# Kernel optimization log

Measured on AMD Instinct MI355X. Metric: run time of the kernel, lower is better.

## Reference

```python
import jax, jax.numpy as jnp
import numpy as np

NODE_DIM = 128
DEPTH = 4
N_NODES = 10000
N_EDGES = 320000


def setup_inputs() -> dict:
    key = jax.random.key(0)
    ks = jax.random.split(key, 12)
    s = 0.05
    D = NODE_DIM
    inp = {
        'h': jax.random.normal(ks[0], (N_NODES, D), jnp.float32),
        'x': jax.random.normal(ks[1], (N_NODES, 3), jnp.float32),
        'edges': jax.random.randint(ks[2], (2, N_EDGES), 0, N_NODES, jnp.int32),
        # edge_mlp: Linear(2D+1 -> D), SiLU, Linear(D -> D), SiLU  (per layer)
        'edge_w1': jax.random.normal(ks[3], (DEPTH, 2 * D + 1, D), jnp.float32) * s,
        'edge_b1': jnp.zeros((DEPTH, D), jnp.float32),
        'edge_w2': jax.random.normal(ks[4], (DEPTH, D, D), jnp.float32) * s,
        'edge_b2': jnp.zeros((DEPTH, D), jnp.float32),
        # node_mlp: Linear(2D -> D), SiLU, Linear(D -> D)  (per layer)
        'node_w1': jax.random.normal(ks[5], (DEPTH, 2 * D, D), jnp.float32) * s,
        'node_b1': jnp.zeros((DEPTH, D), jnp.float32),
        'node_w2': jax.random.normal(ks[6], (DEPTH, D, D), jnp.float32) * s,
        'node_b2': jnp.zeros((DEPTH, D), jnp.float32),
        # coord_mlp (only used by last layer, update_coords=True):
        # Linear(D -> D), SiLU, Linear(D -> 1, bias=False)
        'coord_w1': jax.random.normal(ks[7], (D, D), jnp.float32) * s,
        'coord_b1': jnp.zeros((D,), jnp.float32),
        'coord_w2': jax.random.normal(ks[8], (D, 1), jnp.float32) * s,
    }
    return inp


def reference(h, x, edges, edge_w1, edge_b1, edge_w2, edge_b2,
              node_w1, node_b1, node_w2, node_b2,
              coord_w1, coord_b1, coord_w2):
    silu = jax.nn.silu
    row, col = edges[0], edges[1]
    n = h.shape[0]
    for i in range(DEPTH):
        # coord2radial
        coord_diff = x[row] - x[col]                       # [E, 3]
        radial = jnp.sum(coord_diff * coord_diff, axis=-1, keepdims=True)  # [E, 1]
        # edge_model: m_ij = edge_mlp([h_i, h_j, radial])
        feat = jnp.concatenate([h[row], h[col], radial], axis=-1)  # [E, 2D+1]
        m = silu(feat @ edge_w1[i] + edge_b1[i])
        m = silu(m @ edge_w2[i] + edge_b2[i])              # [E, D]
        # coord_model (only last layer, coords_agg='mean')
        if i == DEPTH - 1:
            w = silu(m @ coord_w1 + coord_b1) @ coord_w2   # [E, 1]
            trans = coord_diff * w                          # [E, 3]
            agg = jax.ops.segment_sum(trans, row, num_segments=n)
            cnt = jax.ops.segment_sum(jnp.ones((row.shape[0], 1), trans.dtype),
                                      row, num_segments=n)
            x = x + agg / jnp.maximum(cnt, 1.0)
        # node_model: h = h + node_mlp([h, sum_j m_ij])  (residual=True)
        magg = jax.ops.segment_sum(m, row, num_segments=n)  # [N, D]
        hin = jnp.concatenate([h, magg], axis=-1)           # [N, 2D]
        out = silu(hin @ node_w1[i] + node_b1[i]) @ node_w2[i] + node_b2[i]
        h = h + out
    return h, x
```

## Files before the change

kernel.cpp:

```cpp
#include <hip/hip_runtime.h>

#define NND 10000
#define NE  320000
#define DD  128
#define NDEPTH 4
#define TE  64

typedef __attribute__((ext_vector_type(8))) short s8b;
typedef __attribute__((ext_vector_type(4))) float f4;
typedef unsigned short u16;
typedef unsigned int   u32;

__device__ __forceinline__ u16 f2b(float f) {
    u32 u = __builtin_bit_cast(u32, f);
    u32 r = (u + 0x7fffu + ((u >> 16) & 1u)) >> 16;
    return (u16)r;
}

__device__ __forceinline__ float b2f(u16 b) {
    u32 u = (u32)b << 16;
    return __builtin_bit_cast(float, u);
}

__device__ __forceinline__ void bpair(u32 v, float& lo, float& hi) {
    lo = __builtin_bit_cast(float, v << 16);
    hi = __builtin_bit_cast(float, v & 0xffff0000u);
}

__device__ __forceinline__ u32 cvt_pk(float lo, float hi) {
    u32 r;
    asm("v_cvt_pk_bf16_f32 %0, %1, %2" : "=v"(r) : "v"(lo), "v"(hi));
    return r;
}

__device__ __forceinline__ u16 f2b1(float v) {
    return (u16)cvt_pk(v, v);
}

__device__ __forceinline__ float silu_f(float v) {
    return v * __builtin_amdgcn_rcpf(1.0f + __expf(-v));
}

__device__ __forceinline__ s8b frag_a(const u16* rowp, int g) {
    union { s8b v; uint2 u2[2]; } r;
    r.u2[0] = *(const uint2*)(rowp + 4 * g);
    r.u2[1] = *(const uint2*)(rowp + 16 + 4 * g);
    return r.v;
}

__device__ __forceinline__ f4 mfma16(s8b a, s8b b, f4 c) {
    return __builtin_amdgcn_mfma_f32_16x16x32_bf16(a, b, c, 0, 0, 0);
}

__global__ __launch_bounds__(256) void egnn_pack(
    const float* __restrict__ ew1, const float* __restrict__ ew2,
    const float* __restrict__ nw1, const float* __restrict__ nw2,
    const float* __restrict__ cw1, u16* __restrict__ pw)
{
    int t = blockIdx.x * 256 + threadIdx.x;
    if (t >= 25 * 16384) return;
    int mat = t >> 14;
    int r   = t & 16383;
    int kt  = r >> 12;
    int nt  = (r >> 9) & 7;
    int lane= (r >> 3) & 63;
    int j   = r & 7;
    int g = lane >> 4, l15 = lane & 15;
    int k = kt * 32 + ((j < 4) ? (4 * g + j) : (16 + 4 * g + (j - 4)));
    int n = nt * 16 + l15;
    float v;
    if (mat < 24) {
        int layer = mat / 6, tp = mat % 6;
        switch (tp) {
            case 0: v = ew1[((size_t)layer * 257 + k) * DD + n]; break;
            case 1: v = ew1[((size_t)layer * 257 + 128 + k) * DD + n]; break;
            case 2: v = ew2[((size_t)layer * 128 + k) * DD + n]; break;
            case 3: v = nw1[((size_t)layer * 256 + k) * DD + n]; break;
            case 4: v = nw1[((size_t)layer * 256 + 128 + k) * DD + n]; break;
            default: v = nw2[((size_t)layer * 128 + k) * DD + n]; break;
        }
    } else {
        v = cw1[(size_t)k * DD + n];
    }
    pw[t] = f2b(v);
}

__global__ __launch_bounds__(256) void egnn_init(
    const float* __restrict__ h, u16* __restrict__ hb)
{
    int i = blockIdx.x * 256 + threadIdx.x;
    size_t base = (size_t)i * 4;
    if (base >= (size_t)NND * DD) return;
    float4 v = *(const float4*)(h + base);
    union { u16 s[4]; uint2 u; } t2;
    t2.s[0] = f2b(v.x); t2.s[1] = f2b(v.y); t2.s[2] = f2b(v.z); t2.s[3] = f2b(v.w);
    *(uint2*)(hb + base) = t2.u;
}

__global__ __launch_bounds__(256) void egnn_count(
    const int* __restrict__ edges, int* __restrict__ cnts)
{
    int e = blockIdx.x * 256 + threadIdx.x;
    if (e < NE) atomicAdd(&cnts[edges[e]], 1);
}

__global__ __launch_bounds__(1024) void egnn_scan(
    const int* __restrict__ cnts, int* __restrict__ off, int* __restrict__ cursor)
{
    __shared__ int part[1024];
    const int t = threadIdx.x;
    const int base = t * 10;
    int s = 0;
    #pragma unroll
    for (int j = 0; j < 10; ++j) {
        int i = base + j;
        s += (i < NND) ? cnts[i] : 0;
    }
    part[t] = s;
    __syncthreads();
    for (int d = 1; d < 1024; d <<= 1) {
        int v = (t >= d) ? part[t - d] : 0;
        __syncthreads();
        part[t] += v;
        __syncthreads();
    }
    int run = (t == 0) ? 0 : part[t - 1];
    #pragma unroll
    for (int j = 0; j < 10; ++j) {
        int i = base + j;
        if (i <= NND) { off[i] = run; cursor[i] = run; }
        if (i < NND) run += cnts[i];
    }
}

__global__ __launch_bounds__(256) void egnn_scatter(
    const int* __restrict__ edges, int* __restrict__ cursor,
    int* __restrict__ rows, int* __restrict__ cols)
{
    int e = blockIdx.x * 256 + threadIdx.x;
    if (e >= NE) return;
    int r = edges[e];
    int p = atomicAdd(&cursor[r], 1);
    rows[p] = r;
    cols[p] = edges[NE + e];
}

__global__ __launch_bounds__(256) void egnn_pre0(
    const u16* __restrict__ hb, const u16* __restrict__ pw,
    const float* __restrict__ eb1,
    float* __restrict__ Pb, u16* __restrict__ Qb)
{
    __shared__ __attribute__((aligned(16))) u16 tH[64][136];
    const int tid = threadIdx.x;
    const int n0  = blockIdx.x * 64;

    #pragma unroll
    for (int it = 0; it < 4; ++it) {
        int idx = tid + it * 256;
        int el = idx >> 4, part = idx & 15;
        int node = n0 + el;
        if (node < NND) {
            *(uint4*)&tH[el][part * 8] = *(const uint4*)(hb + (size_t)node * DD + part * 8);
        } else {
            uint4 z = {0u, 0u, 0u, 0u};
            *(uint4*)&tH[el][part * 8] = z;
        }
    }
    __syncthreads();

    const int wv = tid >> 6, lane = tid & 63;
    const int g = lane >> 4, l15 = lane & 15;
    const int wrow = wv * 16;

    f4 accP[8], accQ[8];
    #pragma unroll
    for (int nt = 0; nt < 8; ++nt) { accP[nt] = f4{0.f,0.f,0.f,0.f}; accQ[nt] = f4{0.f,0.f,0.f,0.f}; }
    const u16* pwa = pw;
    const u16* pwb = pw + 16384;
    #pragma unroll
    for (int kt = 0; kt < 4; ++kt) {
        s8b a = frag_a(&tH[wrow + l15][kt * 32], g);
        const u16* ba = pwa + (size_t)kt * 4096 + lane * 8;
        const u16* bb = pwb + (size_t)kt * 4096 + lane * 8;
        #pragma unroll
        for (int nt = 0; nt < 8; ++nt) {
            accP[nt] = mfma16(a, *(const s8b*)(ba + nt * 512), accP[nt]);
            accQ[nt] = mfma16(a, *(const s8b*)(bb + nt * 512), accQ[nt]);
        }
    }
    #pragma unroll
    for (int nt = 0; nt < 8; ++nt) {
        int n = nt * 16 + l15;
        float bb = eb1[n];
        #pragma unroll
        for (int r = 0; r < 4; ++r) {
            int node = n0 + wrow + g * 4 + r;
            if (node < NND) {
                Pb[(size_t)node * DD + n] = accP[nt][r] + bb;
                Qb[(size_t)node * DD + n] = f2b1(accQ[nt][r]);
            }
        }
    }
}

__global__ __launch_bounds__(256, 6) void egnn_edge(
    const float* __restrict__ Pb, const u16* __restrict__ Qb,
    const float* __restrict__ xin,
    const int* __restrict__ rows, const int* __restrict__ cols,
    const int* __restrict__ off,
    const u16* __restrict__ pw,
    const float* __restrict__ ew1,
    const float* __restrict__ eb2, const float* __restrict__ cb1,
    const float* __restrict__ cw2,
    float* __restrict__ magg, float* __restrict__ aggx,
    int layer, int last)
{
    __shared__ __attribute__((aligned(16))) u16 tA[TE][136];
    __shared__ float rad[TE];
    __shared__ float cdf[TE][3];
    __shared__ int   ridx[TE];
    __shared__ int   cidx[TE];
    __shared__ unsigned char segflag[TE + 1];

    const int tid = threadIdx.x;
    const int nblk = NE / TE;
    const int bid  = blockIdx.x;
    const int blk  = (bid & 7) * (nblk >> 3) + (bid >> 3);
    const int p0   = blk * TE;

    if (tid < TE) {
        int p = p0 + tid;
        int r = rows[p];
        int c = cols[p];
        ridx[tid] = r; cidx[tid] = c;
        float d0 = xin[r * 3 + 0] - xin[c * 3 + 0];
        float d1 = xin[r * 3 + 1] - xin[c * 3 + 1];
        float d2 = xin[r * 3 + 2] - xin[c * 3 + 2];
        rad[tid] = d0 * d0 + d1 * d1 + d2 * d2;
        cdf[tid][0] = d0; cdf[tid][1] = d1; cdf[tid][2] = d2;
    }
    __syncthreads();

    if (tid < TE) {
        segflag[tid] = (tid == 0) || (ridx[tid] != ridx[tid - 1]);
        if (tid == 0) segflag[TE] = 1;
    }

    {
        const int cg = tid & 15;
        const int rg = tid >> 4;
        const float* wrp = ew1 + ((size_t)layer * 257 + 256) * DD + cg * 8;
        float4 w0 = *(const float4*)(wrp);
        float4 w4 = *(const float4*)(wrp + 4);
        #pragma unroll
        for (int k = 0; k < 4; ++k) {
            int row = rg + 16 * k;
            int rn = ridx[row], cn = cidx[row];
            float rd = rad[row];
            const float* pp = Pb + (size_t)rn * DD + cg * 8;
            float4 pa = *(const float4*)(pp);
            float4 pc = *(const float4*)(pp + 4);
            uint4 qv = *(const uint4*)(Qb + (size_t)cn * DD + cg * 8);
            float q0, q1, q2, q3, q4, q5, q6, q7;
            bpair(qv.x, q0, q1);
            bpair(qv.y, q2, q3);
            bpair(qv.z, q4, q5);
            bpair(qv.w, q6, q7);
            float v0 = silu_f(pa.x + q0 + rd * w0.x);
            float v1 = silu_f(pa.y + q1 + rd * w0.y);
            float v2 = silu_f(pa.z + q2 + rd * w0.z);
            float v3 = silu_f(pa.w + q3 + rd * w0.w);
            float v4 = silu_f(pc.x + q4 + rd * w4.x);
            float v5 = silu_f(pc.y + q5 + rd * w4.y);
            float v6 = silu_f(pc.z + q6 + rd * w4.z);
            float v7 = silu_f(pc.w + q7 + rd * w4.w);
            union { u32 w[4]; uint4 u; } cv;
            cv.w[0] = cvt_pk(v0, v1);
            cv.w[1] = cvt_pk(v2, v3);
            cv.w[2] = cvt_pk(v4, v5);
            cv.w[3] = cvt_pk(v6, v7);
            *(uint4*)&tA[row][cg * 8] = cv.u;
        }
    }
    __syncthreads();

    const int wv = tid >> 6, lane = tid & 63;
    const int g = lane >> 4, l15 = lane & 15;
    const int wrow = wv * 16;

    f4 acc2[8];
    #pragma unroll
    for (int nt = 0; nt < 8; ++nt) acc2[nt] = f4{0.f, 0.f, 0.f, 0.f};
    const u16* pw2 = pw + (size_t)(layer * 6 + 2) * 16384;
    #pragma unroll
    for (int kt = 0; kt < 4; ++kt) {
        s8b a = frag_a(&tA[wrow + l15][kt * 32], g);
        const u16* pb = pw2 + (size_t)kt * 4096 + lane * 8;
        #pragma unroll
        for (int nt = 0; nt < 8; ++nt) {
            s8b b = *(const s8b*)(pb + nt * 512);
            acc2[nt] = mfma16(a, b, acc2[nt]);
        }
    }
    {
        const float* b2 = eb2 + (size_t)layer * DD;
        #pragma unroll
        for (int nt = 0; nt < 8; ++nt) {
            int n = nt * 16 + l15;
            float bb = b2[n];
            #pragma unroll
            for (int r = 0; r < 4; ++r) {
                int er = wrow + g * 4 + r;
                float v = silu_f(acc2[nt][r] + bb);
                tA[er][n] = f2b1(v);
            }
        }
    }
    __syncthreads();

    if (tid < 128) {
        int col = tid;
        float s = 0.f;
        int sstart = 0;
        for (int row = 0; row < TE; ++row) {
            s += b2f(tA[row][col]);
            if (segflag[row + 1] || row == TE - 1) {
                int rn = ridx[row];
                bool complete = (p0 + sstart == off[rn]) &&
                                (p0 + row == off[rn + 1] - 1);
                float* mg = &magg[(size_t)rn * DD + col];
                if (complete) *mg = s;
                else          atomicAdd(mg, s);
                s = 0.f;
                sstart = row + 1;
            }
        }
    }

    if (last) {
        f4 acc3[8];
        #pragma unroll
        for (int nt = 0; nt < 8; ++nt) acc3[nt] = f4{0.f, 0.f, 0.f, 0.f};
        const u16* pwc = pw + (size_t)24 * 16384;
        #pragma unroll
        for (int kt = 0; kt < 4; ++kt) {
            s8b a = frag_a(&tA[wrow + l15][kt * 32], g);
            const u16* pb = pwc + (size_t)kt * 4096 + lane * 8;
            #pragma unroll
            for (int nt = 0; nt < 8; ++nt) {
                s8b b = *(const s8b*)(pb + nt * 512);
                acc3[nt] = mfma16(a, b, acc3[nt]);
            }
        }
        float p[4];
        #pragma unroll
        for (int r = 0; r < 4; ++r) p[r] = 0.f;
        #pragma unroll
        for (int nt = 0; nt < 8; ++nt) {
            int n = nt * 16 + l15;
            float bb = cb1[n], w2 = cw2[n];
            #pragma unroll
            for (int r = 0; r < 4; ++r)
                p[r] += silu_f(acc3[nt][r] + bb) * w2;
        }
        #pragma unroll
        for (int o = 1; o < 16; o <<= 1) {
            #pragma unroll
            for (int r = 0; r < 4; ++r)
                p[r] += __shfl_xor(p[r], o);
        }
        if (l15 == 0) {
            #pragma unroll
            for (int r = 0; r < 4; ++r) {
                int er = wrow + 4 * g + r;
                int rn2 = ridx[er];
                float w = p[r];
                atomicAdd(&aggx[rn2 * 3 + 0], cdf[er][0] * w);
                atomicAdd(&aggx[rn2 * 3 + 1], cdf[er][1] * w);
                atomicAdd(&aggx[rn2 * 3 + 2], cdf[er][2] * w);
            }
        }
    }
}

__global__ __launch_bounds__(256) void egnn_node(
    const u16* __restrict__ hb, const float* __restrict__ resid,
    const float* __restrict__ magg, const u16* __restrict__ pw,
    const float* __restrict__ nb1, const float* __restrict__ nb2,
    const float* __restrict__ eb1,
    float* __restrict__ out_h, u16* __restrict__ hb_out,
    float* __restrict__ Pb, u16* __restrict__ Qb,
    int layer, int last)
{
    __shared__ __attribute__((aligned(16))) u16 tH[64][136];
    __shared__ __attribute__((aligned(16))) u16 tM[64][136];
    const int tid = threadIdx.x;
    const int n0  = blockIdx.x * 64;

    #pragma unroll
    for (int it = 0; it < 4; ++it) {
        int idx = tid + it * 256;
        int el = idx >> 4, part = idx & 15;
        int node = n0 + el;
        if (node < NND) {
            *(uint4*)&tH[el][part * 8] = *(const uint4*)(hb + (size_t)node * DD + part * 8);
            const float* ms = magg + (size_t)node * DD + part * 8;
            float4 m0 = *(const float4*)(ms);
            float4 m1 = *(const float4*)(ms + 4);
            union { u32 w[4]; uint4 u; } cv;
            cv.w[0] = cvt_pk(m0.x, m0.y);
            cv.w[1] = cvt_pk(m0.z, m0.w);
            cv.w[2] = cvt_pk(m1.x, m1.y);
            cv.w[3] = cvt_pk(m1.z, m1.w);
            *(uint4*)&tM[el][part * 8] = cv.u;
        } else {
            uint4 z = {0u, 0u, 0u, 0u};
            *(uint4*)&tH[el][part * 8] = z;
            *(uint4*)&tM[el][part * 8] = z;
        }
    }
    __syncthreads();

    const int wv = tid >> 6, lane = tid & 63;
    const int g = lane >> 4, l15 = lane & 15;
    const int wrow = wv * 16;

    f4 acc[8];
    #pragma unroll
    for (int nt = 0; nt < 8; ++nt) acc[nt] = f4{0.f, 0.f, 0.f, 0.f};
    const u16* pn1a = pw + (size_t)(layer * 6 + 3) * 16384;
    const u16* pn1b = pw + (size_t)(layer * 6 + 4) * 16384;
    #pragma unroll
    for (int kt = 0; kt < 8; ++kt) {
        const u16 (*tile)[136] = (kt < 4) ? tH : tM;
        const int k0 = (kt & 3) * 32;
        s8b a = frag_a(&tile[wrow + l15][k0], g);
        const u16* pb = ((kt < 4) ? pn1a : pn1b) + (size_t)(kt & 3) * 4096 + lane * 8;
        #pragma unroll
        for (int nt = 0; nt < 8; ++nt) {
            s8b b = *(const s8b*)(pb + nt * 512);
            acc[nt] = mfma16(a, b, acc[nt]);
        }
    }
    {
        const float* b1 = nb1 + (size_t)layer * DD;
        #pragma unroll
        for (int nt = 0; nt < 8; ++nt) {
            int n = nt * 16 + l15;
            float bb = b1[n];
            #pragma unroll
            for (int r = 0; r < 4; ++r) {
                int er = wrow + g * 4 + r;
                tM[er][n] = f2b1(silu_f(acc[nt][r] + bb));
            }
        }
    }
    __syncthreads();

    f4 acc2[8];
    #pragma unroll
    for (int nt = 0; nt < 8; ++nt) acc2[nt] = f4{0.f, 0.f, 0.f, 0.f};
    const u16* pn2 = pw + (size_t)(layer * 6 + 5) * 16384;
    #pragma unroll
    for (int kt = 0; kt < 4; ++kt) {
        s8b a = frag_a(&tM[wrow + l15][kt * 32], g);
        const u16* pb = pn2 + (size_t)kt * 4096 + lane * 8;
        #pragma unroll
        for (int nt = 0; nt < 8; ++nt) {
            s8b b = *(const s8b*)(pb + nt * 512);
            acc2[nt] = mfma16(a, b, acc2[nt]);
        }
    }
    {
        const float* b2 = nb2 + (size_t)layer * DD;
        #pragma unroll
        for (int nt = 0; nt < 8; ++nt) {
            int n = nt * 16 + l15;
            float bb = b2[n];
            #pragma unroll
            for (int r = 0; r < 4; ++r) {
                int er = wrow + g * 4 + r;
                int node = n0 + er;
                if (node < NND) {
                    float v = acc2[nt][r] + bb + resid[(size_t)node * DD + n];
                    out_h[(size_t)node * DD + n] = v;
                    if (!last) {
                        u16 hv = f2b1(v);
                        hb_out[(size_t)node * DD + n] = hv;
                        tH[er][n] = hv;
                    }
                } else if (!last) {
                    tH[er][n] = 0;
                }
            }
        }
    }

    if (!last) {
        __syncthreads();
        f4 accP[8], accQ[8];
        #pragma unroll
        for (int nt = 0; nt < 8; ++nt) { accP[nt] = f4{0.f,0.f,0.f,0.f}; accQ[nt] = f4{0.f,0.f,0.f,0.f}; }
        const u16* pwa = pw + (size_t)((layer + 1) * 6 + 0) * 16384;
        const u16* pwb = pw + (size_t)((layer + 1) * 6 + 1) * 16384;
        #pragma unroll
        for (int kt = 0; kt < 4; ++kt) {
            s8b a = frag_a(&tH[wrow + l15][kt * 32], g);
            const u16* ba = pwa + (size_t)kt * 4096 + lane * 8;
            const u16* bb = pwb + (size_t)kt * 4096 + lane * 8;
            #pragma unroll
            for (int nt = 0; nt < 8; ++nt) {
                accP[nt] = mfma16(a, *(const s8b*)(ba + nt * 512), accP[nt]);
                accQ[nt] = mfma16(a, *(const s8b*)(bb + nt * 512), accQ[nt]);
            }
        }
        #pragma unroll
        for (int nt = 0; nt < 8; ++nt) {
            int n = nt * 16 + l15;
            float bb = eb1[(size_t)(layer + 1) * DD + n];
            #pragma unroll
            for (int r = 0; r < 4; ++r) {
                int node = n0 + wrow + g * 4 + r;
                if (node < NND) {
                    Pb[(size_t)node * DD + n] = accP[nt][r] + bb;
                    Qb[(size_t)node * DD + n] = f2b1(accQ[nt][r]);
                }
            }
        }
    }
}

__global__ __launch_bounds__(256) void egnn_coord_out(
    const float* __restrict__ xin, const float* __restrict__ aggx,
    const int* __restrict__ off, float* __restrict__ out_x)
{
    int i = blockIdx.x * 256 + threadIdx.x;
    if (i >= NND) return;
    float c = (float)(off[i + 1] - off[i]);
    float inv = 1.0f / fmaxf(c, 1.0f);
    out_x[i * 3 + 0] = xin[i * 3 + 0] + aggx[i * 3 + 0] * inv;
    out_x[i * 3 + 1] = xin[i * 3 + 1] + aggx[i * 3 + 1] * inv;
    out_x[i * 3 + 2] = xin[i * 3 + 2] + aggx[i * 3 + 2] * inv;
}

extern "C" void kernel_launch(void* const* d_in, const int* in_sizes, int n_in,
                              void* d_out, int out_size, void* d_ws, size_t ws_size,
                              hipStream_t stream) {
    const float* h   = (const float*)d_in[0];
    const float* x   = (const float*)d_in[1];
    const int*  edges= (const int*)d_in[2];
    const float* ew1 = (const float*)d_in[3];
    const float* eb1 = (const float*)d_in[4];
    const float* ew2 = (const float*)d_in[5];
    const float* eb2 = (const float*)d_in[6];
    const float* nw1 = (const float*)d_in[7];
    const float* nb1 = (const float*)d_in[8];
    const float* nw2 = (const float*)d_in[9];
    const float* nb2 = (const float*)d_in[10];
    const float* cw1 = (const float*)d_in[11];
    const float* cb1 = (const float*)d_in[12];
    const float* cw2 = (const float*)d_in[13];

    char* ws = (char*)d_ws;
    u16*   hb   = (u16*)  (ws);
    u16*   pw   = (u16*)  (ws + 2560000);
    int*   cnts = (int*)  (ws + 3379200);
    int*   off  = (int*)  (ws + 3419216);
    int*   curs = (int*)  (ws + 3459232);
    int*   rows = (int*)  (ws + 3499248);
    int*   cols = (int*)  (ws + 4779248);
    float* aggx = (float*)(ws + 6059248);
    float* Pb   = (float*)(ws + 6179312);
    u16*   Qb   = (u16*)  (ws + 11299312);
    float* magg = (float*)(ws + 13859312);

    float* out_h = (float*)d_out;
    float* out_x = out_h + (size_t)NND * DD;

    egnn_pack<<<1600, 256, 0, stream>>>(ew1, ew2, nw1, nw2, cw1, pw);
    egnn_init<<<1250, 256, 0, stream>>>(h, hb);
    hipMemsetAsync(aggx, 0, 120064, stream);
    hipMemsetAsync(cnts, 0, 40016, stream);

    egnn_count<<<1250, 256, 0, stream>>>(edges, cnts);
    egnn_scan<<<1, 1024, 0, stream>>>(cnts, off, curs);
    egnn_scatter<<<1250, 256, 0, stream>>>(edges, curs, rows, cols);
    egnn_pre0<<<(NND + 63) / 64, 256, 0, stream>>>(hb, pw, eb1, Pb, Qb);

    for (int i = 0; i < NDEPTH; ++i) {
        int last = (i == NDEPTH - 1);
        hipMemsetAsync(magg, 0, (size_t)NND * DD * 4, stream);
        egnn_edge<<<NE / TE, 256, 0, stream>>>(Pb, Qb, x, rows, cols, off, pw,
                                               ew1, eb2, cb1, cw2,
                                               magg, aggx, i, last);
        const float* resid = (i == 0) ? h : (const float*)out_h;
        egnn_node<<<(NND + 63) / 64, 256, 0, stream>>>(hb, resid, magg, pw, nb1, nb2, eb1,
                                                       out_h, hb, Pb, Qb, i, last);
    }
    egnn_coord_out<<<40, 256, 0, stream>>>(x, aggx, off, out_x);
}
```

Baseline: 510.8 us.

## Replace atomic message aggregation with per-block partial slots summed in node kernel

The edge kernel no longer uses atomicAdd or plain stores into a zeroed magg buffer. Each 64-edge block instead writes its per-node segment sum into a slot indexed by its block offset from the node's first edge, and the node kernel sums those slots while loading. This removes the per-layer memset of magg and the atomic contention on shared nodes. In exchange it assumes no node's edge range spans more than NSLOT=4 blocks, which limits degree to roughly 190. It also enlarges the workspace region needed for partials, and the slot scheme does not enforce either condition.

```diff
diff --git a/kernel.cpp b/kernel.cpp
--- a/kernel.cpp
+++ b/kernel.cpp
@@ -5,6 +5,7 @@
 #define DD  128
 #define NDEPTH 4
 #define TE  64
+#define NSLOT 4
 
 typedef __attribute__((ext_vector_type(8))) short s8b;
 typedef __attribute__((ext_vector_type(4))) float f4;
@@ -212,7 +213,7 @@
     const float* __restrict__ ew1,
     const float* __restrict__ eb2, const float* __restrict__ cb1,
     const float* __restrict__ cw2,
-    float* __restrict__ magg, float* __restrict__ aggx,
+    float* __restrict__ part, float* __restrict__ aggx,
     int layer, int last)
 {
     __shared__ __attribute__((aligned(16))) u16 tA[TE][136];
@@ -321,18 +322,13 @@
     if (tid < 128) {
         int col = tid;
         float s = 0.f;
-        int sstart = 0;
         for (int row = 0; row < TE; ++row) {
             s += b2f(tA[row][col]);
             if (segflag[row + 1] || row == TE - 1) {
                 int rn = ridx[row];
-                bool complete = (p0 + sstart == off[rn]) &&
-                                (p0 + row == off[rn + 1] - 1);
-                float* mg = &magg[(size_t)rn * DD + col];
-                if (complete) *mg = s;
-                else          atomicAdd(mg, s);
+                int slot = blk - (off[rn] >> 6);
+                part[((size_t)rn * NSLOT + slot) * DD + col] = s;
                 s = 0.f;
-                sstart = row + 1;
             }
         }
     }
@@ -385,7 +381,8 @@
 
 __global__ __launch_bounds__(256) void egnn_node(
     const u16* __restrict__ hb, const float* __restrict__ resid,
-    const float* __restrict__ magg, const u16* __restrict__ pw,
+    const float* __restrict__ part, const int* __restrict__ off,
+    const u16* __restrict__ pw,
     const float* __restrict__ nb1, const float* __restrict__ nb2,
     const float* __restrict__ eb1,
     float* __restrict__ out_h, u16* __restrict__ hb_out,
@@ -400,23 +397,34 @@
     #pragma unroll
     for (int it = 0; it < 4; ++it) {
         int idx = tid + it * 256;
-        int el = idx >> 4, part = idx & 15;
+        int el = idx >> 4, pt = idx & 15;
         int node = n0 + el;
         if (node < NND) {
-            *(uint4*)&tH[el][part * 8] = *(const uint4*)(hb + (size_t)node * DD + part * 8);
-            const float* ms = magg + (size_t)node * DD + part * 8;
-            float4 m0 = *(const float4*)(ms);
-            float4 m1 = *(const float4*)(ms + 4);
+            *(uint4*)&tH[el][pt * 8] = *(const uint4*)(hb + (size_t)node * DD + pt * 8);
+            float4 s0 = float4{0.f, 0.f, 0.f, 0.f};
+            float4 s1 = float4{0.f, 0.f, 0.f, 0.f};
+            int a = off[node], b = off[node + 1];
+            if (a < b) {
+                int nsl = ((b - 1) >> 6) - (a >> 6) + 1;
+                const float* pp = part + (size_t)node * NSLOT * DD + pt * 8;
+                for (int t = 0; t < nsl; ++t) {
+                    float4 v0 = *(const float4*)(pp);
+                    float4 v1 = *(const float4*)(pp + 4);
+                    s0.x += v0.x; s0.y += v0.y; s0.z += v0.z; s0.w += v0.w;
+                    s1.x += v1.x; s1.y += v1.y; s1.z += v1.z; s1.w += v1.w;
+                    pp += DD;
+                }
+            }
             union { u32 w[4]; uint4 u; } cv;
-            cv.w[0] = cvt_pk(m0.x, m0.y);
-            cv.w[1] = cvt_pk(m0.z, m0.w);
-            cv.w[2] = cvt_pk(m1.x, m1.y);
-            cv.w[3] = cvt_pk(m1.z, m1.w);
-            *(uint4*)&tM[el][part * 8] = cv.u;
+            cv.w[0] = cvt_pk(s0.x, s0.y);
+            cv.w[1] = cvt_pk(s0.z, s0.w);
+            cv.w[2] = cvt_pk(s1.x, s1.y);
+            cv.w[3] = cvt_pk(s1.z, s1.w);
+            *(uint4*)&tM[el][pt * 8] = cv.u;
         } else {
             uint4 z = {0u, 0u, 0u, 0u};
-            *(uint4*)&tH[el][part * 8] = z;
-            *(uint4*)&tM[el][part * 8] = z;
+            *(uint4*)&tH[el][pt * 8] = z;
+            *(uint4*)&tM[el][pt * 8] = z;
         }
     }
     __syncthreads();
@@ -572,7 +580,7 @@
     float* aggx = (float*)(ws + 6059248);
     float* Pb   = (float*)(ws + 6179312);
     u16*   Qb   = (u16*)  (ws + 11299312);
-    float* magg = (float*)(ws + 13859312);
+    float* part = (float*)(ws + 13859312);
 
     float* out_h = (float*)d_out;
     float* out_x = out_h + (size_t)NND * DD;
@@ -589,12 +597,12 @@
 
     for (int i = 0; i < NDEPTH; ++i) {
         int last = (i == NDEPTH - 1);
-        hipMemsetAsync(magg, 0, (size_t)NND * DD * 4, stream);
         egnn_edge<<<NE / TE, 256, 0, stream>>>(Pb, Qb, x, rows, cols, off, pw,
                                                ew1, eb2, cb1, cw2,
-                                               magg, aggx, i, last);
+                                               part, aggx, i, last);
         const float* resid = (i == 0) ? h : (const float*)out_h;
-        egnn_node<<<(NND + 63) / 64, 256, 0, stream>>>(hb, resid, magg, pw, nb1, nb2, eb1,
+        egnn_node<<<(NND + 63) / 64, 256, 0, stream>>>(hb, resid, part, off,
+                                                       pw, nb1, nb2, eb1,
                                                        out_h, hb, Pb, Qb, i, last);
     }
     egnn_coord_out<<<40, 256, 0, stream>>>(x, aggx, off, out_x);
```

Measured after the change: 477.4 us, median of 2. 6.5% less time.
